# Optimization experiments

Hardware: AMD Instinct MI355X
Metric: run time of the kernel (lower is better)

## Reference

```python
import jax, jax.numpy as jnp
import numpy as np

N, LATENT, K, C = 50000, 16, 16, 64
BATCH = 4
MU = 2.0
HOT_TEMP = 0.01  # sigmoid temperature in hotness()


def _linear_init(key, out_dim, in_dim):
    s = 1.0 / np.sqrt(in_dim)
    kw, kb = jax.random.split(key)
    w = jax.random.uniform(kw, (out_dim, in_dim), jnp.float32, -s, s)
    b = jax.random.uniform(kb, (out_dim,), jnp.float32, -s, s)
    return w, b


def setup_inputs() -> dict:
    key = jax.random.key(0)
    ks = jax.random.split(key, 10)
    x = jax.random.normal(ks[0], (BATCH, N), jnp.float32)
    neighbour_id = jax.random.randint(ks[1], (N, K), 0, N)
    neighbour_distance = jax.random.uniform(ks[2], (N, K), jnp.float32)
    # self-neighbor at distance 0 (as in a real kNN table); keeps window sums > 0
    neighbour_distance = neighbour_distance.at[:, 0].set(0.0)
    clustering_labels = jax.random.randint(ks[3], (N,), 0, C)
    enc1_w, enc1_b = _linear_init(ks[4], 200, N)
    enc2_w, enc2_b = _linear_init(ks[5], LATENT, 200)
    dec_w, dec_b = _linear_init(ks[6], N, LATENT)
    h0_w, h0_b = _linear_init(ks[7], 200, LATENT)
    h1_w, h1_b = _linear_init(ks[8], 200, 200)
    h2_w, h2_b = _linear_init(ks[9], C, 200)
    B = jnp.array([1.0], jnp.float32)  # learnable bandwidth scale, B0=1.0
    return dict(x=x, neighbour_id=neighbour_id, neighbour_distance=neighbour_distance,
                clustering_labels=clustering_labels, enc1_w=enc1_w, enc1_b=enc1_b,
                enc2_w=enc2_w, enc2_b=enc2_b, dec_w=dec_w, dec_b=dec_b,
                h0_w=h0_w, h0_b=h0_b, h1_w=h1_w, h1_b=h1_b, h2_w=h2_w, h2_b=h2_b, B=B)


def reference(x, neighbour_id, neighbour_distance, clustering_labels,
              enc1_w, enc1_b, enc2_w, enc2_b, dec_w, dec_b,
              h0_w, h0_b, h1_w, h1_b, h2_w, h2_b, B):
    # ---- encode: Linear(N,200) -> sigmoid -> Linear(200,n)
    h = jax.nn.sigmoid(x @ enc1_w.T + enc1_b)
    encoded = h @ enc2_w.T + enc2_b                      # [b, n]

    # ---- hotness MLP (SiLU hidden layers, soft sigmoid output), batched over b
    z = encoded @ h0_w.T + h0_b
    z = z * jax.nn.sigmoid(z)
    z = z @ h1_w.T + h1_b
    z = z * jax.nn.sigmoid(z)
    z = z @ h2_w.T + h2_b                                # [b, C]
    H_cluster = jax.nn.sigmoid(HOT_TEMP * z)             # 1/(1+exp(-0.01 z))
    H = H_cluster[:, clustering_labels]                  # [b, N]

    # ---- per-mode bandwidths: (1 - H/2)^i * B,  i = 0..n-1
    powers = jnp.arange(LATENT, dtype=jnp.float32)[:, None]   # [n, 1]
    w = (1.0 - H[:, None, :] / 2.0) ** powers * B[0]          # [b, n, N]

    # ---- bubble window over K neighbours, normalized over K
    d2 = neighbour_distance ** 2                              # [N, K]
    denom = (w * MU) ** 2                                     # [b, n, N]
    win = jax.nn.relu(1.0 - d2[None, None] / denom[..., None])  # [b, n, N, K]
    win = win / jnp.sum(win, axis=-1, keepdims=True)

    # ---- convolve decoder basis (decoder.weight.T is [n, N]) with window
    basis_nbrs = dec_w.T[:, neighbour_id]                     # [n, N, K] gather
    convolved = jnp.einsum('bnik,nik->bni', win, basis_nbrs)  # [b, n, N]

    # ---- decode: bmm(encoded[b,1,n], convolved[b,n,N]) + bias
    out = jnp.einsum('bn,bni->bi', encoded, convolved) + dec_b  # [b, N]
    return out
```

## Files before the change

kernel.cpp:

```cpp
#include <hip/hip_runtime.h>
#include <math.h>

#define NPTS 50000
#define KNBR 16
#define LAT  16
#define NCLS 64
#define NB   4

#define ENC1_CHUNKS 5
#define ENC1_BLOCKS (200 * ENC1_CHUNKS)
#define NLANES (NPTS * 4)
#define CONV_BLOCKS ((NLANES + 255) / 256)

__device__ __forceinline__ float sigmoidf_(float v) { return 1.0f / (1.0f + expf(-v)); }

__global__ __launch_bounds__(256) void k_enc1(const float* __restrict__ x,
                                              const float* __restrict__ w,
                                              float* __restrict__ part) {
  const int NV4 = NPTS / 4;
  const int CV  = NV4 / ENC1_CHUNKS;
  int bid = blockIdx.x;
  int j = bid / ENC1_CHUNKS;
  int chunk = bid - j * ENC1_CHUNKS;
  int t = threadIdx.x;
  const float4* wv = (const float4*)(w + (size_t)j * NPTS);
  const float4* xv = (const float4*)x;
  float a0 = 0.f, a1 = 0.f, a2 = 0.f, a3 = 0.f;
  int vend = (chunk + 1) * CV;
#pragma unroll 2
  for (int v = chunk * CV + t; v < vend; v += 256) {
    float4 wf = wv[v];
    float4 x0 = xv[v];
    float4 x1 = xv[NV4 + v];
    float4 x2 = xv[2 * NV4 + v];
    float4 x3 = xv[3 * NV4 + v];
    a0 += wf.x * x0.x + wf.y * x0.y + wf.z * x0.z + wf.w * x0.w;
    a1 += wf.x * x1.x + wf.y * x1.y + wf.z * x1.z + wf.w * x1.w;
    a2 += wf.x * x2.x + wf.y * x2.y + wf.z * x2.z + wf.w * x2.w;
    a3 += wf.x * x3.x + wf.y * x3.y + wf.z * x3.z + wf.w * x3.w;
  }
#pragma unroll
  for (int off = 32; off > 0; off >>= 1) {
    a0 += __shfl_down(a0, off);
    a1 += __shfl_down(a1, off);
    a2 += __shfl_down(a2, off);
    a3 += __shfl_down(a3, off);
  }
  __shared__ float red[4][4];
  int wid = t >> 6;
  if ((t & 63) == 0) {
    red[wid][0] = a0; red[wid][1] = a1; red[wid][2] = a2; red[wid][3] = a3;
  }
  __syncthreads();
  if (t < 4) {
    float s = red[0][t] + red[1][t] + red[2][t] + red[3][t];
    part[j * 20 + chunk * 4 + t] = s;
  }
}

__global__ __launch_bounds__(1024) void k_mlpABC(const float* __restrict__ part,
                                                 const float* __restrict__ enc1_b,
                                                 const float* __restrict__ enc2_w,
                                                 const float* __restrict__ enc2_b,
                                                 const float* __restrict__ h0_w,
                                                 const float* __restrict__ h0_b,
                                                 float* __restrict__ w_enc,
                                                 float* __restrict__ z0g) {
  __shared__ __align__(16) float4 s_e2w[800];
  __shared__ __align__(16) float s_h0w[200 * 20];
  __shared__ float s_h[NB][200];
  __shared__ float s_enc[NB][LAT];
  int t = threadIdx.x;

  if (t < 800) {
    float4 we = ((const float4*)enc2_w)[t];
    float4 wh = ((const float4*)h0_w)[t];
    s_e2w[t] = we;
    int jo = t >> 2, c = t & 3;
    *(float4*)&s_h0w[jo * 20 + c * 4] = wh;
  }

  if (t < 800) {
    int j = t >> 2, b = t & 3;
    float v = part[j * 20 + 0 + b] + part[j * 20 + 4 + b] + part[j * 20 + 8 + b] +
              part[j * 20 + 12 + b] + part[j * 20 + 16 + b] + enc1_b[j];
    s_h[b][j] = sigmoidf_(v);
  }
  __syncthreads();

  {
    int g = t >> 4, p = t & 15;
    int b = g >> 4, i = g & 15;
    float s = 0.f;
    for (int f = p; f < 50; f += 16) {
      float4 w = s_e2w[i * 50 + f];
      int j = f * 4;
      s += w.x * s_h[b][j] + w.y * s_h[b][j + 1] + w.z * s_h[b][j + 2] + w.w * s_h[b][j + 3];
    }
    s += __shfl_xor(s, 1, 16);
    s += __shfl_xor(s, 2, 16);
    s += __shfl_xor(s, 4, 16);
    s += __shfl_xor(s, 8, 16);
    if (p == 0) {
      s += enc2_b[i];
      s_enc[b][i] = s;
      w_enc[b * LAT + i] = s;
    }
  }
  __syncthreads();

  if (t < 800) {
    int jo = t >> 2, b = t & 3;
    const float* hw = &s_h0w[jo * 20];
    float4 w0 = *(const float4*)&hw[0];
    float4 w1 = *(const float4*)&hw[4];
    float4 w2 = *(const float4*)&hw[8];
    float4 w3 = *(const float4*)&hw[12];
    float s = h0_b[jo];
    s += w0.x * s_enc[b][0] + w0.y * s_enc[b][1] + w0.z * s_enc[b][2] + w0.w * s_enc[b][3];
    s += w1.x * s_enc[b][4] + w1.y * s_enc[b][5] + w1.z * s_enc[b][6] + w1.w * s_enc[b][7];
    s += w2.x * s_enc[b][8] + w2.y * s_enc[b][9] + w2.z * s_enc[b][10] + w2.w * s_enc[b][11];
    s += w3.x * s_enc[b][12] + w3.y * s_enc[b][13] + w3.z * s_enc[b][14] + w3.w * s_enc[b][15];
    z0g[jo * 4 + b] = s * sigmoidf_(s);
  }
}

__global__ __launch_bounds__(256) void k_mlpD(const float* __restrict__ z0g,
                                              const float* __restrict__ h1_w,
                                              const float* __restrict__ h1_b,
                                              float* __restrict__ z1g) {
  __shared__ __align__(16) float4 s_z0[200];
  int t = threadIdx.x;
  for (int o = t; o < 200; o += 256) s_z0[o] = ((const float4*)z0g)[o];
  __syncthreads();

  int row = blockIdx.x * 4 + (t >> 6);
  int l = t & 63;
  float d0 = 0.f, d1 = 0.f, d2 = 0.f, d3 = 0.f;
  if (l < 50) {
    float4 w = ((const float4*)(h1_w + row * 200))[l];
    float4 z0 = s_z0[4 * l + 0], z1 = s_z0[4 * l + 1];
    float4 z2 = s_z0[4 * l + 2], z3 = s_z0[4 * l + 3];
    d0 = w.x * z0.x + w.y * z1.x + w.z * z2.x + w.w * z3.x;
    d1 = w.x * z0.y + w.y * z1.y + w.z * z2.y + w.w * z3.y;
    d2 = w.x * z0.z + w.y * z1.z + w.z * z2.z + w.w * z3.z;
    d3 = w.x * z0.w + w.y * z1.w + w.z * z2.w + w.w * z3.w;
  }
#pragma unroll
  for (int m = 32; m > 0; m >>= 1) {
    d0 += __shfl_xor(d0, m, 64);
    d1 += __shfl_xor(d1, m, 64);
    d2 += __shfl_xor(d2, m, 64);
    d3 += __shfl_xor(d3, m, 64);
  }
  if (l == 0) {
    float bb = h1_b[row];
    float s;
    s = d0 + bb; z1g[row * 4 + 0] = s * sigmoidf_(s);
    s = d1 + bb; z1g[row * 4 + 1] = s * sigmoidf_(s);
    s = d2 + bb; z1g[row * 4 + 2] = s * sigmoidf_(s);
    s = d3 + bb; z1g[row * 4 + 3] = s * sigmoidf_(s);
  }
}

__global__ __launch_bounds__(256) void k_mlpE(const float* __restrict__ z1g,
                                              const float* __restrict__ h2_w,
                                              const float* __restrict__ h2_b,
                                              float* __restrict__ w_hcl) {
  __shared__ __align__(16) float4 s_z1[200];
  int t = threadIdx.x;
  for (int o = t; o < 200; o += 256) s_z1[o] = ((const float4*)z1g)[o];
  __syncthreads();

  int c = blockIdx.x * 4 + (t >> 6);
  int l = t & 63;
  float e0 = 0.f, e1 = 0.f, e2 = 0.f, e3 = 0.f;
  if (l < 50) {
    float4 w = ((const float4*)(h2_w + c * 200))[l];
    float4 za = s_z1[4 * l + 0], zb = s_z1[4 * l + 1];
    float4 zc = s_z1[4 * l + 2], zd = s_z1[4 * l + 3];
    e0 = w.x * za.x + w.y * zb.x + w.z * zc.x + w.w * zd.x;
    e1 = w.x * za.y + w.y * zb.y + w.z * zc.y + w.w * zd.y;
    e2 = w.x * za.z + w.y * zb.z + w.z * zc.z + w.w * zd.z;
    e3 = w.x * za.w + w.y * zb.w + w.z * zc.w + w.w * zd.w;
  }
#pragma unroll
  for (int m = 32; m > 0; m >>= 1) {
    e0 += __shfl_xor(e0, m, 64);
    e1 += __shfl_xor(e1, m, 64);
    e2 += __shfl_xor(e2, m, 64);
    e3 += __shfl_xor(e3, m, 64);
  }
  if (l == 0) {
    float sb = h2_b[c];
    w_hcl[0 * NCLS + c] = sigmoidf_(0.01f * (e0 + sb));
    w_hcl[1 * NCLS + c] = sigmoidf_(0.01f * (e1 + sb));
    w_hcl[2 * NCLS + c] = sigmoidf_(0.01f * (e2 + sb));
    w_hcl[3 * NCLS + c] = sigmoidf_(0.01f * (e3 + sb));
  }
}

__global__ __launch_bounds__(256, 4) void k_conv(const int* __restrict__ nid,
                                                 const float* __restrict__ nd,
                                                 const int* __restrict__ labels,
                                                 const float* __restrict__ dec_w,
                                                 const float* __restrict__ dec_b,
                                                 const float* __restrict__ Bp,
                                                 const float* __restrict__ w_enc,
                                                 const float* __restrict__ w_hcl,
                                                 float* __restrict__ out) {
  __shared__ float s_enc[NB * LAT];
  __shared__ float s_hcl[NB * NCLS];
  int t = threadIdx.x;
  if (t < NB * LAT) s_enc[t] = w_enc[t];
  s_hcl[t] = w_hcl[t];
  __syncthreads();

  int gidx = blockIdx.x * 256 + t;
  int n = gidx >> 2;
  int q = t & 3;
  if (n >= NPTS) return;

  const float4* nd4 = (const float4*)nd + (size_t)n * 4;
  const int4*   ni4 = (const int4*)nid + (size_t)n * 4;
  float dA[16];
  int nA[16];
#pragma unroll
  for (int a = 0; a < 4; ++a) {
    float4 v = nd4[a];
    int4  iv = ni4[a];
    dA[a * 4 + 0] = v.x * v.x; dA[a * 4 + 1] = v.y * v.y;
    dA[a * 4 + 2] = v.z * v.z; dA[a * 4 + 3] = v.w * v.w;
    nA[a * 4 + 0] = iv.x; nA[a * 4 + 1] = iv.y;
    nA[a * 4 + 2] = iv.z; nA[a * 4 + 3] = iv.w;
  }

  int lab = labels[n];
  float decb = dec_b[n];
  float Bv = Bp[0];

  const float4* dw4 = (const float4*)dec_w;
  float4 dwp[8];
#pragma unroll
  for (int k = 0; k < 8; ++k)
    dwp[k] = dw4[(size_t)nA[k] * 4 + q];

  float inv0 = 1.0f / (4.0f * Bv * Bv);

  float ivd[4][4];
#pragma unroll
  for (int b = 0; b < 4; ++b) {
    float H = s_hcl[b * NCLS + lab];
    float base = 1.0f - 0.5f * H;
    float rb = __builtin_amdgcn_rcpf(base * base);
    float rb2 = rb * rb;
    float rb4 = rb2 * rb2;
    float rb8 = rb4 * rb4;
    float start = inv0;
    if (q & 1) start *= rb4;
    if (q & 2) start *= rb8;
    ivd[b][0] = start;
    ivd[b][1] = ivd[b][0] * rb;
    ivd[b][2] = ivd[b][1] * rb;
    ivd[b][3] = ivd[b][2] * rb;
  }

  float sden[4][4], num[4][4];
#pragma unroll
  for (int b = 0; b < 4; ++b)
#pragma unroll
    for (int j = 0; j < 4; ++j) { sden[b][j] = 0.f; num[b][j] = 0.f; }

#pragma unroll
  for (int k = 0; k < KNBR; ++k) {
    float4 dw = (k < 8) ? dwp[k] : dw4[(size_t)nA[k] * 4 + q];
    float d2k = dA[k];
#pragma unroll
    for (int b = 0; b < 4; ++b) {
      float w0 = fmaxf(fmaf(-d2k, ivd[b][0], 1.0f), 0.0f);
      float w1 = fmaxf(fmaf(-d2k, ivd[b][1], 1.0f), 0.0f);
      float w2 = fmaxf(fmaf(-d2k, ivd[b][2], 1.0f), 0.0f);
      float w3 = fmaxf(fmaf(-d2k, ivd[b][3], 1.0f), 0.0f);
      sden[b][0] += w0; num[b][0] = fmaf(w0, dw.x, num[b][0]);
      sden[b][1] += w1; num[b][1] = fmaf(w1, dw.y, num[b][1]);
      sden[b][2] += w2; num[b][2] = fmaf(w2, dw.z, num[b][2]);
      sden[b][3] += w3; num[b][3] = fmaf(w3, dw.w, num[b][3]);
    }
  }

  float acc[4];
#pragma unroll
  for (int b = 0; b < 4; ++b) {
    float a = 0.f;
#pragma unroll
    for (int j = 0; j < 4; ++j) {
      a = fmaf(s_enc[b * LAT + q * 4 + j] * __builtin_amdgcn_rcpf(sden[b][j]),
               num[b][j], a);
    }
    acc[b] = a;
  }

  float tA = (q & 1) ? acc[0] : acc[2];
  float tB = (q & 1) ? acc[1] : acc[3];
  float rA = __shfl_xor(tA, 1, 4);
  float rB = __shfl_xor(tB, 1, 4);
  float u = (q & 1) ? (acc[2] + rA) : (acc[0] + rA);
  float v = (q & 1) ? (acc[3] + rB) : (acc[1] + rB);
  float tC = (q & 2) ? u : v;
  float rC = __shfl_xor(tC, 2, 4);
  float f = (q & 2) ? (v + rC) : (u + rC);
  int bmap = ((q & 1) << 1) | ((q & 2) >> 1);
  out[(size_t)bmap * NPTS + n] = f + decb;
}

extern "C" void kernel_launch(void* const* d_in, const int* in_sizes, int n_in,
                              void* d_out, int out_size, void* d_ws, size_t ws_size,
                              hipStream_t stream) {
  const float* x      = (const float*)d_in[0];
  const int*   nid    = (const int*)d_in[1];
  const float* nd     = (const float*)d_in[2];
  const int*   labels = (const int*)d_in[3];
  const float* enc1_w = (const float*)d_in[4];
  const float* enc1_b = (const float*)d_in[5];
  const float* enc2_w = (const float*)d_in[6];
  const float* enc2_b = (const float*)d_in[7];
  const float* dec_w  = (const float*)d_in[8];
  const float* dec_b  = (const float*)d_in[9];
  const float* h0_w   = (const float*)d_in[10];
  const float* h0_b   = (const float*)d_in[11];
  const float* h1_w   = (const float*)d_in[12];
  const float* h1_b   = (const float*)d_in[13];
  const float* h2_w   = (const float*)d_in[14];
  const float* h2_b   = (const float*)d_in[15];
  const float* Bp     = (const float*)d_in[16];
  float* out = (float*)d_out;
  float* ws  = (float*)d_ws;
  float* part  = ws;
  float* w_enc = ws + 4000;
  float* w_hcl = ws + 4064;
  float* z0g   = ws + 4320;
  float* z1g   = ws + 5120;

  k_enc1<<<ENC1_BLOCKS, 256, 0, stream>>>(x, enc1_w, part);
  k_mlpABC<<<1, 1024, 0, stream>>>(part, enc1_b, enc2_w, enc2_b, h0_w, h0_b,
                                   w_enc, z0g);
  k_mlpD<<<50, 256, 0, stream>>>(z0g, h1_w, h1_b, z1g);
  k_mlpE<<<16, 256, 0, stream>>>(z1g, h2_w, h2_b, w_hcl);
  k_conv<<<CONV_BLOCKS, 256, 0, stream>>>(nid, nd, labels, dec_w, dec_b,
                                          Bp, w_enc, w_hcl, out);
}
```

Before: 37.07 us.

## Fuse three MLP kernels into one using grid-wide atomic barriers

Replaces the three separate MLP kernels (enc2/h0, h1, h2) with a single 50-block kernel that synchronises its stages through global atomic counters reset by a memset. The h1 and h2 weight rows are prefetched into registers before the first barrier, so their loads overlap block 0's serial enc2/h0 work. The aim is to remove two kernel launch gaps from a latency-bound chain. In exchange it adds a memset launch and spin-wait barriers, and it relies on all 50 blocks being resident at the same time.

New measurement: 47.35 us. 1.28x slower.

```diff
diff --git a/kernel.cpp b/kernel.cpp
--- a/kernel.cpp
+++ b/kernel.cpp
@@ -11,6 +11,7 @@
 #define ENC1_BLOCKS (200 * ENC1_CHUNKS)
 #define NLANES (NPTS * 4)
 #define CONV_BLOCKS ((NLANES + 255) / 256)
+#define MLP_BLOCKS 50
 
 __device__ __forceinline__ float sigmoidf_(float v) { return 1.0f / (1.0f + expf(-v)); }
 
@@ -58,145 +59,165 @@
   }
 }
 
-__global__ __launch_bounds__(1024) void k_mlpABC(const float* __restrict__ part,
-                                                 const float* __restrict__ enc1_b,
-                                                 const float* __restrict__ enc2_w,
-                                                 const float* __restrict__ enc2_b,
-                                                 const float* __restrict__ h0_w,
-                                                 const float* __restrict__ h0_b,
-                                                 float* __restrict__ w_enc,
-                                                 float* __restrict__ z0g) {
+__global__ __launch_bounds__(256) void k_mlpFused(
+    const float* __restrict__ part,
+    const float* __restrict__ enc1_b,
+    const float* __restrict__ enc2_w,
+    const float* __restrict__ enc2_b,
+    const float* __restrict__ h0_w,
+    const float* __restrict__ h0_b,
+    const float* __restrict__ h1_w,
+    const float* __restrict__ h1_b,
+    const float* __restrict__ h2_w,
+    const float* __restrict__ h2_b,
+    float* __restrict__ w_enc,
+    float* __restrict__ w_hcl,
+    float* __restrict__ z0g,
+    float* __restrict__ z1g,
+    unsigned int* __restrict__ bar1,
+    unsigned int* __restrict__ bar2)
+{
   __shared__ __align__(16) float4 s_e2w[800];
   __shared__ __align__(16) float s_h0w[200 * 20];
   __shared__ float s_h[NB][200];
   __shared__ float s_enc[NB][LAT];
-  int t = threadIdx.x;
-
-  if (t < 800) {
-    float4 we = ((const float4*)enc2_w)[t];
-    float4 wh = ((const float4*)h0_w)[t];
-    s_e2w[t] = we;
-    int jo = t >> 2, c = t & 3;
-    *(float4*)&s_h0w[jo * 20 + c * 4] = wh;
-  }
-
-  if (t < 800) {
-    int j = t >> 2, b = t & 3;
-    float v = part[j * 20 + 0 + b] + part[j * 20 + 4 + b] + part[j * 20 + 8 + b] +
-              part[j * 20 + 12 + b] + part[j * 20 + 16 + b] + enc1_b[j];
-    s_h[b][j] = sigmoidf_(v);
-  }
-  __syncthreads();
-
+  __shared__ __align__(16) float4 s_z0[200];
+  __shared__ __align__(16) float4 s_z1[200];
+
+  int t = threadIdx.x, bid = blockIdx.x;
+  int wv = t >> 6, l = t & 63;
+  int row = bid * 4 + wv;
+
+  float4 wD = make_float4(0.f, 0.f, 0.f, 0.f);
+  float4 wE = make_float4(0.f, 0.f, 0.f, 0.f);
+  if (l < 50) wD = ((const float4*)(h1_w + row * 200))[l];
+  if (bid < 16 && l < 50) wE = ((const float4*)(h2_w + row * 200))[l];
+
+  if (bid == 0) {
+    for (int o = t; o < 800; o += 256) {
+      float4 we = ((const float4*)enc2_w)[o];
+      float4 wh = ((const float4*)h0_w)[o];
+      s_e2w[o] = we;
+      int jo = o >> 2, c = o & 3;
+      *(float4*)&s_h0w[jo * 20 + c * 4] = wh;
+    }
+    for (int o = t; o < 800; o += 256) {
+      int j = o >> 2, b = o & 3;
+      float v = part[j * 20 + 0 + b] + part[j * 20 + 4 + b] + part[j * 20 + 8 + b] +
+                part[j * 20 + 12 + b] + part[j * 20 + 16 + b] + enc1_b[j];
+      s_h[b][j] = sigmoidf_(v);
+    }
+    __syncthreads();
+    {
+      int g = t >> 2, p = t & 3;
+      int b = g >> 4, i = g & 15;
+      float s = 0.f;
+      for (int f = p; f < 50; f += 4) {
+        float4 w = s_e2w[i * 50 + f];
+        int j = f * 4;
+        s += w.x * s_h[b][j] + w.y * s_h[b][j + 1] + w.z * s_h[b][j + 2] + w.w * s_h[b][j + 3];
+      }
+      s += __shfl_xor(s, 1, 4);
+      s += __shfl_xor(s, 2, 4);
+      if (p == 0) {
+        s += enc2_b[i];
+        s_enc[b][i] = s;
+        w_enc[b * LAT + i] = s;
+      }
+    }
+    __syncthreads();
+    for (int o = t; o < 800; o += 256) {
+      int jo = o >> 2, b = o & 3;
+      const float* hw = &s_h0w[jo * 20];
+      float4 w0 = *(const float4*)&hw[0];
+      float4 w1 = *(const float4*)&hw[4];
+      float4 w2 = *(const float4*)&hw[8];
+      float4 w3 = *(const float4*)&hw[12];
+      float s = h0_b[jo];
+      s += w0.x * s_enc[b][0] + w0.y * s_enc[b][1] + w0.z * s_enc[b][2] + w0.w * s_enc[b][3];
+      s += w1.x * s_enc[b][4] + w1.y * s_enc[b][5] + w1.z * s_enc[b][6] + w1.w * s_enc[b][7];
+      s += w2.x * s_enc[b][8] + w2.y * s_enc[b][9] + w2.z * s_enc[b][10] + w2.w * s_enc[b][11];
+      s += w3.x * s_enc[b][12] + w3.y * s_enc[b][13] + w3.z * s_enc[b][14] + w3.w * s_enc[b][15];
+      z0g[jo * 4 + b] = s * sigmoidf_(s);
+    }
+  }
+
+  if (t == 0) {
+    __threadfence();
+    __hip_atomic_fetch_add(bar1, 1u, __ATOMIC_ACQ_REL, __HIP_MEMORY_SCOPE_AGENT);
+    while (__hip_atomic_load(bar1, __ATOMIC_RELAXED, __HIP_MEMORY_SCOPE_AGENT) < (unsigned)MLP_BLOCKS)
+      __builtin_amdgcn_s_sleep(1);
+    (void)__hip_atomic_load(bar1, __ATOMIC_ACQUIRE, __HIP_MEMORY_SCOPE_AGENT);
+  }
+  __syncthreads();
+
+  if (t < 200) s_z0[t] = ((const float4*)z0g)[t];
+  __syncthreads();
   {
-    int g = t >> 4, p = t & 15;
-    int b = g >> 4, i = g & 15;
-    float s = 0.f;
-    for (int f = p; f < 50; f += 16) {
-      float4 w = s_e2w[i * 50 + f];
-      int j = f * 4;
-      s += w.x * s_h[b][j] + w.y * s_h[b][j + 1] + w.z * s_h[b][j + 2] + w.w * s_h[b][j + 3];
-    }
-    s += __shfl_xor(s, 1, 16);
-    s += __shfl_xor(s, 2, 16);
-    s += __shfl_xor(s, 4, 16);
-    s += __shfl_xor(s, 8, 16);
-    if (p == 0) {
-      s += enc2_b[i];
-      s_enc[b][i] = s;
-      w_enc[b * LAT + i] = s;
-    }
-  }
-  __syncthreads();
-
-  if (t < 800) {
-    int jo = t >> 2, b = t & 3;
-    const float* hw = &s_h0w[jo * 20];
-    float4 w0 = *(const float4*)&hw[0];
-    float4 w1 = *(const float4*)&hw[4];
-    float4 w2 = *(const float4*)&hw[8];
-    float4 w3 = *(const float4*)&hw[12];
-    float s = h0_b[jo];
-    s += w0.x * s_enc[b][0] + w0.y * s_enc[b][1] + w0.z * s_enc[b][2] + w0.w * s_enc[b][3];
-    s += w1.x * s_enc[b][4] + w1.y * s_enc[b][5] + w1.z * s_enc[b][6] + w1.w * s_enc[b][7];
-    s += w2.x * s_enc[b][8] + w2.y * s_enc[b][9] + w2.z * s_enc[b][10] + w2.w * s_enc[b][11];
-    s += w3.x * s_enc[b][12] + w3.y * s_enc[b][13] + w3.z * s_enc[b][14] + w3.w * s_enc[b][15];
-    z0g[jo * 4 + b] = s * sigmoidf_(s);
-  }
-}
-
-__global__ __launch_bounds__(256) void k_mlpD(const float* __restrict__ z0g,
-                                              const float* __restrict__ h1_w,
-                                              const float* __restrict__ h1_b,
-                                              float* __restrict__ z1g) {
-  __shared__ __align__(16) float4 s_z0[200];
-  int t = threadIdx.x;
-  for (int o = t; o < 200; o += 256) s_z0[o] = ((const float4*)z0g)[o];
-  __syncthreads();
-
-  int row = blockIdx.x * 4 + (t >> 6);
-  int l = t & 63;
-  float d0 = 0.f, d1 = 0.f, d2 = 0.f, d3 = 0.f;
-  if (l < 50) {
-    float4 w = ((const float4*)(h1_w + row * 200))[l];
-    float4 z0 = s_z0[4 * l + 0], z1 = s_z0[4 * l + 1];
-    float4 z2 = s_z0[4 * l + 2], z3 = s_z0[4 * l + 3];
-    d0 = w.x * z0.x + w.y * z1.x + w.z * z2.x + w.w * z3.x;
-    d1 = w.x * z0.y + w.y * z1.y + w.z * z2.y + w.w * z3.y;
-    d2 = w.x * z0.z + w.y * z1.z + w.z * z2.z + w.w * z3.z;
-    d3 = w.x * z0.w + w.y * z1.w + w.z * z2.w + w.w * z3.w;
-  }
-#pragma unroll
-  for (int m = 32; m > 0; m >>= 1) {
-    d0 += __shfl_xor(d0, m, 64);
-    d1 += __shfl_xor(d1, m, 64);
-    d2 += __shfl_xor(d2, m, 64);
-    d3 += __shfl_xor(d3, m, 64);
-  }
-  if (l == 0) {
-    float bb = h1_b[row];
-    float s;
-    s = d0 + bb; z1g[row * 4 + 0] = s * sigmoidf_(s);
-    s = d1 + bb; z1g[row * 4 + 1] = s * sigmoidf_(s);
-    s = d2 + bb; z1g[row * 4 + 2] = s * sigmoidf_(s);
-    s = d3 + bb; z1g[row * 4 + 3] = s * sigmoidf_(s);
-  }
-}
-
-__global__ __launch_bounds__(256) void k_mlpE(const float* __restrict__ z1g,
-                                              const float* __restrict__ h2_w,
-                                              const float* __restrict__ h2_b,
-                                              float* __restrict__ w_hcl) {
-  __shared__ __align__(16) float4 s_z1[200];
-  int t = threadIdx.x;
-  for (int o = t; o < 200; o += 256) s_z1[o] = ((const float4*)z1g)[o];
-  __syncthreads();
-
-  int c = blockIdx.x * 4 + (t >> 6);
-  int l = t & 63;
-  float e0 = 0.f, e1 = 0.f, e2 = 0.f, e3 = 0.f;
-  if (l < 50) {
-    float4 w = ((const float4*)(h2_w + c * 200))[l];
-    float4 za = s_z1[4 * l + 0], zb = s_z1[4 * l + 1];
-    float4 zc = s_z1[4 * l + 2], zd = s_z1[4 * l + 3];
-    e0 = w.x * za.x + w.y * zb.x + w.z * zc.x + w.w * zd.x;
-    e1 = w.x * za.y + w.y * zb.y + w.z * zc.y + w.w * zd.y;
-    e2 = w.x * za.z + w.y * zb.z + w.z * zc.z + w.w * zd.z;
-    e3 = w.x * za.w + w.y * zb.w + w.z * zc.w + w.w * zd.w;
-  }
-#pragma unroll
-  for (int m = 32; m > 0; m >>= 1) {
-    e0 += __shfl_xor(e0, m, 64);
-    e1 += __shfl_xor(e1, m, 64);
-    e2 += __shfl_xor(e2, m, 64);
-    e3 += __shfl_xor(e3, m, 64);
-  }
-  if (l == 0) {
-    float sb = h2_b[c];
-    w_hcl[0 * NCLS + c] = sigmoidf_(0.01f * (e0 + sb));
-    w_hcl[1 * NCLS + c] = sigmoidf_(0.01f * (e1 + sb));
-    w_hcl[2 * NCLS + c] = sigmoidf_(0.01f * (e2 + sb));
-    w_hcl[3 * NCLS + c] = sigmoidf_(0.01f * (e3 + sb));
+    float d0 = 0.f, d1 = 0.f, d2 = 0.f, d3 = 0.f;
+    if (l < 50) {
+      float4 z0 = s_z0[4 * l + 0], z1 = s_z0[4 * l + 1];
+      float4 z2 = s_z0[4 * l + 2], z3 = s_z0[4 * l + 3];
+      d0 = wD.x * z0.x + wD.y * z1.x + wD.z * z2.x + wD.w * z3.x;
+      d1 = wD.x * z0.y + wD.y * z1.y + wD.z * z2.y + wD.w * z3.y;
+      d2 = wD.x * z0.z + wD.y * z1.z + wD.z * z2.z + wD.w * z3.z;
+      d3 = wD.x * z0.w + wD.y * z1.w + wD.z * z2.w + wD.w * z3.w;
+    }
+#pragma unroll
+    for (int m = 32; m > 0; m >>= 1) {
+      d0 += __shfl_xor(d0, m, 64);
+      d1 += __shfl_xor(d1, m, 64);
+      d2 += __shfl_xor(d2, m, 64);
+      d3 += __shfl_xor(d3, m, 64);
+    }
+    if (l == 0) {
+      float bb = h1_b[row];
+      float s;
+      s = d0 + bb; z1g[row * 4 + 0] = s * sigmoidf_(s);
+      s = d1 + bb; z1g[row * 4 + 1] = s * sigmoidf_(s);
+      s = d2 + bb; z1g[row * 4 + 2] = s * sigmoidf_(s);
+      s = d3 + bb; z1g[row * 4 + 3] = s * sigmoidf_(s);
+    }
+  }
+
+  if (t == 0) {
+    __threadfence();
+    __hip_atomic_fetch_add(bar2, 1u, __ATOMIC_ACQ_REL, __HIP_MEMORY_SCOPE_AGENT);
+  }
+  if (bid >= 16) return;
+  if (t == 0) {
+    while (__hip_atomic_load(bar2, __ATOMIC_RELAXED, __HIP_MEMORY_SCOPE_AGENT) < (unsigned)MLP_BLOCKS)
+      __builtin_amdgcn_s_sleep(1);
+    (void)__hip_atomic_load(bar2, __ATOMIC_ACQUIRE, __HIP_MEMORY_SCOPE_AGENT);
+  }
+  __syncthreads();
+
+  if (t < 200) s_z1[t] = ((const float4*)z1g)[t];
+  __syncthreads();
+  {
+    float e0 = 0.f, e1 = 0.f, e2 = 0.f, e3 = 0.f;
+    if (l < 50) {
+      float4 za = s_z1[4 * l + 0], zb = s_z1[4 * l + 1];
+      float4 zc = s_z1[4 * l + 2], zd = s_z1[4 * l + 3];
+      e0 = wE.x * za.x + wE.y * zb.x + wE.z * zc.x + wE.w * zd.x;
+      e1 = wE.x * za.y + wE.y * zb.y + wE.z * zc.y + wE.w * zd.y;
+      e2 = wE.x * za.z + wE.y * zb.z + wE.z * zc.z + wE.w * zd.z;
+      e3 = wE.x * za.w + wE.y * zb.w + wE.z * zc.w + wE.w * zd.w;
+    }
+#pragma unroll
+    for (int m = 32; m > 0; m >>= 1) {
+      e0 += __shfl_xor(e0, m, 64);
+      e1 += __shfl_xor(e1, m, 64);
+      e2 += __shfl_xor(e2, m, 64);
+      e3 += __shfl_xor(e3, m, 64);
+    }
+    if (l == 0) {
+      float sb = h2_b[row];
+      w_hcl[0 * NCLS + row] = sigmoidf_(0.01f * (e0 + sb));
+      w_hcl[1 * NCLS + row] = sigmoidf_(0.01f * (e1 + sb));
+      w_hcl[2 * NCLS + row] = sigmoidf_(0.01f * (e2 + sb));
+      w_hcl[3 * NCLS + row] = sigmoidf_(0.01f * (e3 + sb));
+    }
   }
 }
 
@@ -340,12 +361,14 @@
   float* w_hcl = ws + 4064;
   float* z0g   = ws + 4320;
   float* z1g   = ws + 5120;
-
+  unsigned int* bars = (unsigned int*)(ws + 5920);
+
+  hipMemsetAsync(bars, 0, 8, stream);
   k_enc1<<<ENC1_BLOCKS, 256, 0, stream>>>(x, enc1_w, part);
-  k_mlpABC<<<1, 1024, 0, stream>>>(part, enc1_b, enc2_w, enc2_b, h0_w, h0_b,
-                                   w_enc, z0g);
-  k_mlpD<<<50, 256, 0, stream>>>(z0g, h1_w, h1_b, z1g);
-  k_mlpE<<<16, 256, 0, stream>>>(z1g, h2_w, h2_b, w_hcl);
+  k_mlpFused<<<MLP_BLOCKS, 256, 0, stream>>>(part, enc1_b, enc2_w, enc2_b,
+                                             h0_w, h0_b, h1_w, h1_b, h2_w, h2_b,
+                                             w_enc, w_hcl, z0g, z1g,
+                                             bars, bars + 1);
   k_conv<<<CONV_BLOCKS, 256, 0, stream>>>(nid, nd, labels, dec_w, dec_b,
                                           Bp, w_enc, w_hcl, out);
 }
```
